# Performance work log

Measured on AMD Instinct MI355X. Metric: run time of the kernel, lower is better.

The kernel has to match this reference:

```python
import jax, jax.numpy as jnp
import numpy as np

DIM = 1024
HEADS = 16
HEAD_DIM = DIM // HEADS
WINDOW = 128


def setup_inputs() -> dict:
    key = jax.random.key(0)
    k1, k2, k3, k4 = jax.random.split(key, 4)
    B, T = 2, 2048
    x = jax.random.normal(k1, (B, T, DIM), dtype=jnp.float32)
    # nn.Linear(dim, 3*dim, bias=False): weight [3*dim, dim]; y = x @ W.T
    W_qkv = jax.random.normal(k2, (3 * DIM, DIM), dtype=jnp.float32) * (1.0 / np.sqrt(DIM))
    W_proj = jax.random.normal(k3, (DIM, DIM), dtype=jnp.float32) * (1.0 / np.sqrt(DIM))
    b_proj = jax.random.normal(k4, (DIM,), dtype=jnp.float32) * 0.01
    return {"x": x, "W_qkv": W_qkv, "W_proj": W_proj, "b_proj": b_proj}


def reference(x, W_qkv, W_proj, b_proj) -> jnp.ndarray:
    B, T, C = x.shape
    scale = HEAD_DIM ** -0.5
    qkv = jnp.einsum('btc,oc->bto', x, W_qkv)  # [B,T,3*D]
    qkv = qkv.reshape(B, T, 3, HEADS, HEAD_DIM)
    qkv = jnp.transpose(qkv, (2, 0, 3, 1, 4))  # [3,B,H,T,hd]
    q, k, v = qkv[0], qkv[1], qkv[2]
    # sliding-window mask: attend iff |i-j| <= WINDOW
    idx = jnp.arange(T)
    mask = jnp.abs(idx[:, None] - idx[None, :]) <= WINDOW  # [T,T]
    scores = jnp.einsum('bhqd,bhkd->bhqk', q, k) * scale  # [B,H,T,T]
    scores = jnp.where(mask[None, None], scores, jnp.finfo(scores.dtype).min)
    attn = jax.nn.softmax(scores, axis=-1)
    out = jnp.einsum('bhqk,bhkd->bhqd', attn, v)  # [B,H,T,hd]
    out = jnp.transpose(out, (0, 2, 1, 3)).reshape(B, T, C)
    return jnp.einsum('btc,oc->bto', out, W_proj) + b_proj
```

## Files before the change

kernel.cpp:

```cpp
#include <hip/hip_runtime.h>
#include <hip/hip_bf16.h>
#include <cstdint>
#include <cstddef>

#define DIMC 1024
#define HEADS 16
#define HD 64
#define WINDOW 128
#define BB 2
#define TT 2048
#define NTOK (BB*TT)
#define QKVN (3*DIMC)

typedef __bf16 bf16;
typedef __bf16 bf16x8 __attribute__((ext_vector_type(8)));
typedef __bf16 bf16x4 __attribute__((ext_vector_type(4)));
typedef float f32x4 __attribute__((ext_vector_type(4)));
typedef unsigned int u32;

typedef const __attribute__((address_space(1))) u32* gp1_t;
typedef __attribute__((address_space(3))) u32* lp3_t;

__device__ __forceinline__ void gload16(const void* g, void* l) {
  __builtin_amdgcn_global_load_lds((gp1_t)g, (lp3_t)l, 16, 0, 0);
}

__device__ __forceinline__ u32 lds_u32(const void* p) {
  return (u32)(uintptr_t)(__attribute__((address_space(3))) const void*)p;
}

__device__ __forceinline__ void BAR() {
  asm volatile("" ::: "memory");
  __builtin_amdgcn_s_barrier();
  asm volatile("" ::: "memory");
}

__global__ void cast3_kernel(const float* __restrict__ x,
                             const float* __restrict__ wq,
                             const float* __restrict__ wp,
                             bf16* __restrict__ xo,
                             bf16* __restrict__ wqo,
                             bf16* __restrict__ wpo) {
  const int NX = NTOK * DIMC / 4;
  const int NQ = QKVN * DIMC / 4;
  const int NP = DIMC * DIMC / 4;
  const int total = NX + NQ + NP;
  typedef float float4v __attribute__((ext_vector_type(4)));
  for (int i = blockIdx.x * blockDim.x + threadIdx.x; i < total;
       i += gridDim.x * blockDim.x) {
    const float4v* src; bf16* dst; int j;
    if (i < NX)            { src = (const float4v*)x;  dst = xo;  j = i; }
    else if (i < NX + NQ)  { src = (const float4v*)wq; dst = wqo; j = i - NX; }
    else                   { src = (const float4v*)wp; dst = wpo; j = i - NX - NQ; }
    float4v v = src[j];
    bf16x4 o;
    o[0] = (bf16)v[0]; o[1] = (bf16)v[1]; o[2] = (bf16)v[2]; o[3] = (bf16)v[3];
    ((bf16x4*)dst)[j] = o;
  }
}

__device__ __forceinline__ bf16x8 lds_frag(const bf16* base, int row, int colb) {
  const char* p = (const char*)base + row * 128 + (colb ^ ((row & 7) << 4));
  return *(const bf16x8*)p;
}

__global__ __launch_bounds__(512, 2) void gemm_qkv_kernel(
    const bf16* __restrict__ A, const bf16* __restrict__ Bw,
    bf16* __restrict__ C) {
  constexpr int NT = 16;
  __shared__ bf16 Al[2][128 * 64];
  __shared__ bf16 Bl[2][192 * 64];

  const int tid = threadIdx.x;
  const int w = tid >> 6, l = tid & 63;
  const int wm = w >> 2, wn = w & 3;
  const int lr = l & 15, lg = l >> 4;

  const int bid = blockIdx.x;
  const int x = bid & 7, i = bid >> 3;
  const int bm = 8 * (x >> 1) + (i & 7);
  const int bn = 8 * (x & 1) + (i >> 3);

  const char* Ag = (const char*)A + (size_t)(bm * 128) * 2048;
  const char* Bg = (const char*)Bw + (size_t)(bn * 192) * 2048;

  auto stageA = [&](bf16* lds, int kt) {
#pragma unroll
    for (int i2 = 0; i2 < 2; i2++) {
      const int R0 = w * 16 + i2 * 8;
      const int r = R0 + (l >> 3);
      const char* src = Ag + (size_t)r * 2048 + kt * 128
                        + (((l & 7) * 16) ^ ((r & 7) << 4));
      gload16(src, lds + R0 * 64);
    }
  };
  auto stageB = [&](bf16* lds, int kt) {
#pragma unroll
    for (int i2 = 0; i2 < 3; i2++) {
      const int R0 = w * 24 + i2 * 8;
      const int r = R0 + (l >> 3);
      const char* src = Bg + (size_t)r * 2048 + kt * 128
                        + (((l & 7) * 16) ^ ((r & 7) << 4));
      gload16(src, lds + R0 * 64);
    }
  };

  stageA(Al[0], 0); stageB(Bl[0], 0);
  stageA(Al[1], 1); stageB(Bl[1], 1);
  asm volatile("s_waitcnt vmcnt(5)" ::: "memory");
  BAR();

  f32x4 acc[4][3] = {};

  for (int kt = 0; kt < NT; ++kt) {
    const bf16* Ac = Al[kt & 1];
    const bf16* Bc = Bl[kt & 1];

    bf16x8 af[4][2], bf[3][2];
#pragma unroll
    for (int m = 0; m < 4; m++)
#pragma unroll
      for (int kk = 0; kk < 2; kk++)
        af[m][kk] = lds_frag(Ac, wm * 64 + m * 16 + lr, kk * 64 + lg * 16);
#pragma unroll
    for (int n = 0; n < 3; n++)
#pragma unroll
      for (int kk = 0; kk < 2; kk++)
        bf[n][kk] = lds_frag(Bc, wn * 48 + n * 16 + lr, kk * 64 + lg * 16);

    asm volatile("s_waitcnt lgkmcnt(0)" ::: "memory");
    __builtin_amdgcn_sched_barrier(0);
    BAR();

    if (kt + 2 < NT) {
      stageA(Al[kt & 1], kt + 2);
      stageB(Bl[kt & 1], kt + 2);
    }

    __builtin_amdgcn_s_setprio(1);
#pragma unroll
    for (int kk = 0; kk < 2; kk++)
#pragma unroll
      for (int m = 0; m < 4; m++)
#pragma unroll
        for (int n = 0; n < 3; n++)
          acc[m][n] = __builtin_amdgcn_mfma_f32_16x16x32_bf16(
              af[m][kk], bf[n][kk], acc[m][n], 0, 0, 0);
    __builtin_amdgcn_s_setprio(0);

    if (kt < NT - 2) asm volatile("s_waitcnt vmcnt(5)" ::: "memory");
    else             asm volatile("s_waitcnt vmcnt(0)" ::: "memory");
    BAR();
  }

#pragma unroll
  for (int m = 0; m < 4; m++) {
    const int row = bm * 128 + wm * 64 + m * 16 + lg * 4;
#pragma unroll
    for (int n = 0; n < 3; n++) {
      const int col = bn * 192 + wn * 48 + n * 16 + lr;
#pragma unroll
      for (int j = 0; j < 4; j++)
        C[(size_t)(row + j) * QKVN + col] = (bf16)acc[m][n][j];
    }
  }
}

__global__ __launch_bounds__(512, 2) void gemm_proj_kernel(
    const bf16* __restrict__ A, const bf16* __restrict__ Bw,
    float* __restrict__ Cf, const float* __restrict__ bias) {
  constexpr int NT = 16;
  __shared__ bf16 Al[2][128 * 64];
  __shared__ bf16 Bl[2][64 * 64];

  const int tid = threadIdx.x;
  const int w = tid >> 6, l = tid & 63;
  const int wm = w >> 1, wn = w & 1;
  const int lr = l & 15, lg = l >> 4;

  const int bid = blockIdx.x;
  const int x = bid & 7, i = bid >> 3;
  const int bm = 8 * (x >> 1) + (i & 7);
  const int bn = 8 * (x & 1) + (i >> 3);

  const char* Ag = (const char*)A + (size_t)(bm * 128) * 2048;
  const char* Bg = (const char*)Bw + (size_t)(bn * 64) * 2048;

  auto stageA = [&](bf16* lds, int kt) {
#pragma unroll
    for (int i2 = 0; i2 < 2; i2++) {
      const int R0 = w * 16 + i2 * 8;
      const int r = R0 + (l >> 3);
      const char* src = Ag + (size_t)r * 2048 + kt * 128
                        + (((l & 7) * 16) ^ ((r & 7) << 4));
      gload16(src, lds + R0 * 64);
    }
  };
  auto stageB = [&](bf16* lds, int kt) {
    const int R0 = w * 8;
    const int r = R0 + (l >> 3);
    const char* src = Bg + (size_t)r * 2048 + kt * 128
                      + (((l & 7) * 16) ^ ((r & 7) << 4));
    gload16(src, lds + R0 * 64);
  };

  stageA(Al[0], 0); stageB(Bl[0], 0);
  stageA(Al[1], 1); stageB(Bl[1], 1);
  asm volatile("s_waitcnt vmcnt(3)" ::: "memory");
  BAR();

  f32x4 acc[2][2] = {};

  for (int kt = 0; kt < NT; ++kt) {
    const bf16* Ac = Al[kt & 1];
    const bf16* Bc = Bl[kt & 1];

    bf16x8 af[2][2], bf[2][2];
#pragma unroll
    for (int m = 0; m < 2; m++)
#pragma unroll
      for (int kk = 0; kk < 2; kk++)
        af[m][kk] = lds_frag(Ac, wm * 32 + m * 16 + lr, kk * 64 + lg * 16);
#pragma unroll
    for (int n = 0; n < 2; n++)
#pragma unroll
      for (int kk = 0; kk < 2; kk++)
        bf[n][kk] = lds_frag(Bc, wn * 32 + n * 16 + lr, kk * 64 + lg * 16);

    asm volatile("s_waitcnt lgkmcnt(0)" ::: "memory");
    __builtin_amdgcn_sched_barrier(0);
    BAR();

    if (kt + 2 < NT) {
      stageA(Al[kt & 1], kt + 2);
      stageB(Bl[kt & 1], kt + 2);
    }

    __builtin_amdgcn_s_setprio(1);
#pragma unroll
    for (int kk = 0; kk < 2; kk++)
#pragma unroll
      for (int m = 0; m < 2; m++)
#pragma unroll
        for (int n = 0; n < 2; n++)
          acc[m][n] = __builtin_amdgcn_mfma_f32_16x16x32_bf16(
              af[m][kk], bf[n][kk], acc[m][n], 0, 0, 0);
    __builtin_amdgcn_s_setprio(0);

    if (kt < NT - 2) asm volatile("s_waitcnt vmcnt(3)" ::: "memory");
    else             asm volatile("s_waitcnt vmcnt(0)" ::: "memory");
    BAR();
  }

#pragma unroll
  for (int m = 0; m < 2; m++) {
    const int row = bm * 128 + wm * 32 + m * 16 + lg * 4;
#pragma unroll
    for (int n = 0; n < 2; n++) {
      const int col = bn * 64 + wn * 32 + n * 16 + lr;
#pragma unroll
      for (int j = 0; j < 4; j++)
        Cf[(size_t)(row + j) * DIMC + col] = acc[m][n][j] + bias[col];
    }
  }
}

__global__ __launch_bounds__(512, 4) void attn_kernel(const bf16* __restrict__ qkv,
                                                      bf16* __restrict__ out) {
  __shared__ bf16 Kl[3][64 * 64];
  __shared__ bf16 Vl[3][64 * 64];

  const int tid = threadIdx.x, w = tid >> 6, l = tid & 63;
  const int bid = blockIdx.x;
  const int x = bid & 7, ii = bid >> 3;
  const int bh = x * 4 + (ii >> 4);
  const int qb = ii & 15;
  const int b = bh >> 4, h = bh & 15;
  const int q0 = qb * 128;
  const int lr = l & 15, lg = l >> 4;
  const float SC = 0.18033688011f;

  const char* qkv_b = (const char*)qkv + (size_t)(b * TT) * (QKVN * 2);

  size_t koff; u32 kdst;
  {
    const int R0 = 8 * w;
    const int r = R0 + (l >> 3);
    const int colb = (((l & 7) * 16) ^ (((l >> 3) & 7) << 4));
    koff = (size_t)r * (QKVN * 2) + (DIMC + h * HD) * 2 + colb;
    kdst = (u32)(R0 * 64);
  }
  size_t voff; u32 vdst;
  {
    const int c = tid;
    const int t = c >> 3, w_ = c & 7;
    const int kv = (t & 15) * 4 + (w_ >> 1);
    const int d  = (t >> 4) * 16 + (w_ & 1) * 8;
    voff = (size_t)kv * (QKVN * 2) + (2 * DIMC + h * HD + d) * 2;
    vdst = (u32)(w * 512);
  }

  auto stage = [&](int buf, int kb) {
    const char* rowb = qkv_b + (size_t)(kb * 64) * (QKVN * 2);
    gload16(rowb + koff, &Kl[buf][kdst]);
    gload16(rowb + voff, &Vl[buf][vdst]);
  };

  bf16x8 qf[2];
  {
    const bf16* qp = qkv + (size_t)(b * TT + q0 + w * 16 + lr) * QKVN + h * HD + lg * 8;
    qf[0] = *(const bf16x8*)qp;
    qf[1] = *(const bf16x8*)(qp + 32);
  }

  f32x4 Oa[4] = {};
  float mrow = -1e30f, lrow = 0.f;

  int kb0 = 2 * qb - 2; if (kb0 < 0) kb0 = 0;
  int kb1 = 2 * qb + 3; if (kb1 > 31) kb1 = 31;

  stage(0, kb0);
  stage(1, kb0 + 1);
  asm volatile("s_waitcnt vmcnt(2)" ::: "memory");
  BAR();

  for (int kb = kb0; kb <= kb1; ++kb) {
    const int c = (kb - kb0) % 3;
    if (kb + 2 <= kb1) stage((c + 2) % 3, kb + 2);

    const bf16* Kb = &Kl[c][0];
    f32x4 Sa[4] = {};
#pragma unroll
    for (int kf = 0; kf < 2; kf++)
#pragma unroll
      for (int nf = 0; nf < 4; nf++) {
        const char* kp = (const char*)Kb + (nf * 16 + lr) * 128
                         + ((kf * 64 + lg * 16) ^ ((lr & 7) << 4));
        bf16x8 kfr = *(const bf16x8*)kp;
        Sa[nf] = __builtin_amdgcn_mfma_f32_16x16x32_bf16(kfr, qf[kf], Sa[nf], 0, 0, 0);
      }

    bf16x4 tr0[4][2], tr1[4][2];
    {
      const u32 vbase = lds_u32(&Vl[c][0]) + l * 8;
#pragma unroll
      for (int nf = 0; nf < 4; nf++)
#pragma unroll
        for (int kf = 0; kf < 2; kf++) {
          const u32 a = vbase + (u32)((nf * 16 + kf * 8) * 128);
          asm volatile("ds_read_b64_tr_b16 %0, %1"
                       : "=v"(tr0[nf][kf]) : "v"(a));
          asm volatile("ds_read_b64_tr_b16 %0, %1 offset:512"
                       : "=v"(tr1[nf][kf]) : "v"(a));
        }
    }

    const int kvb = kb * 64;
    const int qrow = q0 + w * 16 + lr;
    float mblk = -1e30f;
#pragma unroll
    for (int nf = 0; nf < 4; nf++)
#pragma unroll
      for (int j = 0; j < 4; j++) {
        int kv = kvb + nf * 16 + lg * 4 + j;
        int dq = qrow - kv;
        float s = Sa[nf][j] * SC;
        if (dq > WINDOW || dq < -WINDOW) s = -1e30f;
        Sa[nf][j] = s;
        mblk = fmaxf(mblk, s);
      }
    mblk = fmaxf(mblk, __shfl_xor(mblk, 16));
    mblk = fmaxf(mblk, __shfl_xor(mblk, 32));

    if (!__all(mblk <= mrow + 8.f)) {
      float mn = fmaxf(mrow, mblk);
      float sc = exp2f(mrow - mn);
      mrow = mn;
      lrow *= sc;
#pragma unroll
      for (int j = 0; j < 4; j++) {
        float so = __shfl(sc, lg * 4 + j);
#pragma unroll
        for (int nf = 0; nf < 4; nf++) Oa[nf][j] *= so;
      }
    }

    float rsum = 0.f;
#pragma unroll
    for (int nf = 0; nf < 4; nf++)
#pragma unroll
      for (int j = 0; j < 4; j++) {
        float e = exp2f(Sa[nf][j] - mrow);
        Sa[nf][j] = e;
        rsum += e;
      }
    rsum += __shfl_xor(rsum, 16);
    rsum += __shfl_xor(rsum, 32);
    lrow += rsum;

    bf16x8 pa[2];
#pragma unroll
    for (int kf = 0; kf < 2; kf++)
#pragma unroll
      for (int e = 0; e < 4; e++) {
        pa[kf][e]     = (bf16)Sa[2 * kf][e];
        pa[kf][e + 4] = (bf16)Sa[2 * kf + 1][e];
      }

    asm volatile("s_waitcnt lgkmcnt(0)" ::: "memory");
    __builtin_amdgcn_sched_barrier(0);
#pragma unroll
    for (int nf = 0; nf < 4; nf++)
#pragma unroll
      for (int kf = 0; kf < 2; kf++) {
        bf16x8 vb;
#pragma unroll
        for (int e = 0; e < 4; e++) {
          vb[e]     = tr0[nf][kf][e];
          vb[e + 4] = tr1[nf][kf][e];
        }
        Oa[nf] = __builtin_amdgcn_mfma_f32_16x16x32_bf16(pa[kf], vb, Oa[nf], 0, 0, 0);
      }

    if (kb < kb1) {
      if (kb + 2 <= kb1) asm volatile("s_waitcnt vmcnt(2)" ::: "memory");
      else               asm volatile("s_waitcnt vmcnt(0)" ::: "memory");
    }
    BAR();
  }

  float lo[4];
#pragma unroll
  for (int j = 0; j < 4; j++) lo[j] = __shfl(lrow, lg * 4 + j);
#pragma unroll
  for (int nf = 0; nf < 4; nf++) {
#pragma unroll
    for (int j = 0; j < 4; j++) {
      int q = q0 + w * 16 + lg * 4 + j;
      int d = nf * 16 + lr;
      out[(size_t)(b * TT + q) * DIMC + h * HD + d] = (bf16)(Oa[nf][j] / lo[j]);
    }
  }
}

extern "C" void kernel_launch(void* const* d_in, const int* in_sizes, int n_in,
                              void* d_out, int out_size, void* d_ws, size_t ws_size,
                              hipStream_t stream) {
  const float* x     = (const float*)d_in[0];
  const float* Wqkv  = (const float*)d_in[1];
  const float* Wproj = (const float*)d_in[2];
  const float* bproj = (const float*)d_in[3];
  float* out = (float*)d_out;

  char* ws = (char*)d_ws;
  bf16* xb   = (bf16*)(ws);
  bf16* wqb  = (bf16*)(ws + 8388608);
  bf16* wpb  = (bf16*)(ws + 14680064);
  bf16* qkvb = (bf16*)(ws + 16777216);
  bf16* aob  = (bf16*)(ws + 41943040);

  cast3_kernel<<<2048, 256, 0, stream>>>(x, Wqkv, Wproj, xb, wqb, wpb);
  gemm_qkv_kernel<<<512, 512, 0, stream>>>(xb, wqb, qkvb);
  attn_kernel<<<512, 512, 0, stream>>>(qkvb, aob);
  gemm_proj_kernel<<<512, 512, 0, stream>>>(aob, wpb, out, bproj);
}
```

Measured before the change: 76.02 us.

## Fuse weight fp32-to-bf16 conversion into GEMM B-tile loading

The separate cast kernel now converts only x. Both GEMMs load fp32 weight tiles into registers, convert them to bf16 and write them swizzled into LDS, with the next tile's global load issued during the current MFMA phase. This removes a cast pass over 16 MB of fp32 weights and the bf16 weight buffers, but each weight tile is now read as fp32 by many blocks. It also adds register pressure and replaces the async global_load_lds path for B with an explicit register round-trip and different vmcnt waits.

```diff
diff --git a/kernel.cpp b/kernel.cpp
--- a/kernel.cpp
+++ b/kernel.cpp
@@ -16,6 +16,7 @@
 typedef __bf16 bf16x8 __attribute__((ext_vector_type(8)));
 typedef __bf16 bf16x4 __attribute__((ext_vector_type(4)));
 typedef float f32x4 __attribute__((ext_vector_type(4)));
+typedef float float4v __attribute__((ext_vector_type(4)));
 typedef unsigned int u32;
 
 typedef const __attribute__((address_space(1))) u32* gp1_t;
@@ -35,27 +36,15 @@
   asm volatile("" ::: "memory");
 }
 
-__global__ void cast3_kernel(const float* __restrict__ x,
-                             const float* __restrict__ wq,
-                             const float* __restrict__ wp,
-                             bf16* __restrict__ xo,
-                             bf16* __restrict__ wqo,
-                             bf16* __restrict__ wpo) {
+__global__ void castx_kernel(const float* __restrict__ x,
+                             bf16* __restrict__ xo) {
   const int NX = NTOK * DIMC / 4;
-  const int NQ = QKVN * DIMC / 4;
-  const int NP = DIMC * DIMC / 4;
-  const int total = NX + NQ + NP;
-  typedef float float4v __attribute__((ext_vector_type(4)));
-  for (int i = blockIdx.x * blockDim.x + threadIdx.x; i < total;
+  for (int i = blockIdx.x * blockDim.x + threadIdx.x; i < NX;
        i += gridDim.x * blockDim.x) {
-    const float4v* src; bf16* dst; int j;
-    if (i < NX)            { src = (const float4v*)x;  dst = xo;  j = i; }
-    else if (i < NX + NQ)  { src = (const float4v*)wq; dst = wqo; j = i - NX; }
-    else                   { src = (const float4v*)wp; dst = wpo; j = i - NX - NQ; }
-    float4v v = src[j];
+    float4v v = ((const float4v*)x)[i];
     bf16x4 o;
     o[0] = (bf16)v[0]; o[1] = (bf16)v[1]; o[2] = (bf16)v[2]; o[3] = (bf16)v[3];
-    ((bf16x4*)dst)[j] = o;
+    ((bf16x4*)xo)[i] = o;
   }
 }
 
@@ -65,7 +54,7 @@
 }
 
 __global__ __launch_bounds__(512, 2) void gemm_qkv_kernel(
-    const bf16* __restrict__ A, const bf16* __restrict__ Bw,
+    const bf16* __restrict__ A, const float* __restrict__ Wq,
     bf16* __restrict__ C) {
   constexpr int NT = 16;
   __shared__ bf16 Al[2][128 * 64];
@@ -82,7 +71,7 @@
   const int bn = 8 * (x & 1) + (i >> 3);
 
   const char* Ag = (const char*)A + (size_t)(bm * 128) * 2048;
-  const char* Bg = (const char*)Bw + (size_t)(bn * 192) * 2048;
+  const float* Bg = Wq + (size_t)(bn * 192) * 1024;
 
   auto stageA = [&](bf16* lds, int kt) {
 #pragma unroll
@@ -94,20 +83,37 @@
       gload16(src, lds + R0 * 64);
     }
   };
-  auto stageB = [&](bf16* lds, int kt) {
+
+  float br[24];
+  auto loadB = [&](int kt) {
 #pragma unroll
     for (int i2 = 0; i2 < 3; i2++) {
-      const int R0 = w * 24 + i2 * 8;
-      const int r = R0 + (l >> 3);
-      const char* src = Bg + (size_t)r * 2048 + kt * 128
-                        + (((l & 7) * 16) ^ ((r & 7) << 4));
-      gload16(src, lds + R0 * 64);
-    }
-  };
-
-  stageA(Al[0], 0); stageB(Bl[0], 0);
-  stageA(Al[1], 1); stageB(Bl[1], 1);
-  asm volatile("s_waitcnt vmcnt(5)" ::: "memory");
+      const int r = w * 24 + i2 * 8 + (l >> 3);
+      const float* src = Bg + (size_t)r * 1024 + kt * 64 + (l & 7) * 8;
+      float4v v0 = *(const float4v*)src;
+      float4v v1 = *(const float4v*)(src + 4);
+#pragma unroll
+      for (int e = 0; e < 4; e++) { br[i2 * 8 + e] = v0[e]; br[i2 * 8 + 4 + e] = v1[e]; }
+    }
+  };
+  auto writeB = [&](bf16* lds) {
+#pragma unroll
+    for (int i2 = 0; i2 < 3; i2++) {
+      const int r = w * 24 + i2 * 8 + (l >> 3);
+      bf16x8 o;
+#pragma unroll
+      for (int e = 0; e < 8; e++) o[e] = (bf16)br[i2 * 8 + e];
+      *(bf16x8*)((char*)lds + r * 128 + (((l & 7) * 16) ^ ((r & 7) << 4))) = o;
+    }
+  };
+
+  loadB(0);
+  stageA(Al[0], 0); stageA(Al[1], 1);
+  asm volatile("s_waitcnt vmcnt(4)" ::: "memory");
+  writeB(Bl[0]);
+  loadB(1);
+  asm volatile("s_waitcnt vmcnt(8)" ::: "memory");
+  asm volatile("s_waitcnt lgkmcnt(0)" ::: "memory");
   BAR();
 
   f32x4 acc[4][3] = {};
@@ -132,10 +138,13 @@
     __builtin_amdgcn_sched_barrier(0);
     BAR();
 
-    if (kt + 2 < NT) {
-      stageA(Al[kt & 1], kt + 2);
-      stageB(Bl[kt & 1], kt + 2);
-    }
+    if (kt + 2 < NT) stageA(Al[kt & 1], kt + 2);
+    if (kt + 1 < NT) {
+      if (kt + 2 < NT) asm volatile("s_waitcnt vmcnt(2)" ::: "memory");
+      else             asm volatile("s_waitcnt vmcnt(0)" ::: "memory");
+      writeB(Bl[(kt + 1) & 1]);
+    }
+    if (kt + 2 < NT) loadB(kt + 2);
 
     __builtin_amdgcn_s_setprio(1);
 #pragma unroll
@@ -148,8 +157,7 @@
               af[m][kk], bf[n][kk], acc[m][n], 0, 0, 0);
     __builtin_amdgcn_s_setprio(0);
 
-    if (kt < NT - 2) asm volatile("s_waitcnt vmcnt(5)" ::: "memory");
-    else             asm volatile("s_waitcnt vmcnt(0)" ::: "memory");
+    asm volatile("s_waitcnt lgkmcnt(0)" ::: "memory");
     BAR();
   }
 
@@ -167,7 +175,7 @@
 }
 
 __global__ __launch_bounds__(512, 2) void gemm_proj_kernel(
-    const bf16* __restrict__ A, const bf16* __restrict__ Bw,
+    const bf16* __restrict__ A, const float* __restrict__ Wp,
     float* __restrict__ Cf, const float* __restrict__ bias) {
   constexpr int NT = 16;
   __shared__ bf16 Al[2][128 * 64];
@@ -184,7 +192,7 @@
   const int bn = 8 * (x & 1) + (i >> 3);
 
   const char* Ag = (const char*)A + (size_t)(bm * 128) * 2048;
-  const char* Bg = (const char*)Bw + (size_t)(bn * 64) * 2048;
+  const float* Bg = Wp + (size_t)(bn * 64) * 1024;
 
   auto stageA = [&](bf16* lds, int kt) {
 #pragma unroll
@@ -196,17 +204,31 @@
       gload16(src, lds + R0 * 64);
     }
   };
-  auto stageB = [&](bf16* lds, int kt) {
-    const int R0 = w * 8;
-    const int r = R0 + (l >> 3);
-    const char* src = Bg + (size_t)r * 2048 + kt * 128
-                      + (((l & 7) * 16) ^ ((r & 7) << 4));
-    gload16(src, lds + R0 * 64);
-  };
-
-  stageA(Al[0], 0); stageB(Bl[0], 0);
-  stageA(Al[1], 1); stageB(Bl[1], 1);
-  asm volatile("s_waitcnt vmcnt(3)" ::: "memory");
+
+  float br[8];
+  auto loadB = [&](int kt) {
+    const int r = w * 8 + (l >> 3);
+    const float* src = Bg + (size_t)r * 1024 + kt * 64 + (l & 7) * 8;
+    float4v v0 = *(const float4v*)src;
+    float4v v1 = *(const float4v*)(src + 4);
+#pragma unroll
+    for (int e = 0; e < 4; e++) { br[e] = v0[e]; br[4 + e] = v1[e]; }
+  };
+  auto writeB = [&](bf16* lds) {
+    const int r = w * 8 + (l >> 3);
+    bf16x8 o;
+#pragma unroll
+    for (int e = 0; e < 8; e++) o[e] = (bf16)br[e];
+    *(bf16x8*)((char*)lds + r * 128 + (((l & 7) * 16) ^ ((r & 7) << 4))) = o;
+  };
+
+  loadB(0);
+  stageA(Al[0], 0); stageA(Al[1], 1);
+  asm volatile("s_waitcnt vmcnt(4)" ::: "memory");
+  writeB(Bl[0]);
+  loadB(1);
+  asm volatile("s_waitcnt vmcnt(4)" ::: "memory");
+  asm volatile("s_waitcnt lgkmcnt(0)" ::: "memory");
   BAR();
 
   f32x4 acc[2][2] = {};
@@ -231,10 +253,13 @@
     __builtin_amdgcn_sched_barrier(0);
     BAR();
 
-    if (kt + 2 < NT) {
-      stageA(Al[kt & 1], kt + 2);
-      stageB(Bl[kt & 1], kt + 2);
-    }
+    if (kt + 2 < NT) stageA(Al[kt & 1], kt + 2);
+    if (kt + 1 < NT) {
+      if (kt + 2 < NT) asm volatile("s_waitcnt vmcnt(2)" ::: "memory");
+      else             asm volatile("s_waitcnt vmcnt(0)" ::: "memory");
+      writeB(Bl[(kt + 1) & 1]);
+    }
+    if (kt + 2 < NT) loadB(kt + 2);
 
     __builtin_amdgcn_s_setprio(1);
 #pragma unroll
@@ -247,8 +272,7 @@
               af[m][kk], bf[n][kk], acc[m][n], 0, 0, 0);
     __builtin_amdgcn_s_setprio(0);
 
-    if (kt < NT - 2) asm volatile("s_waitcnt vmcnt(3)" ::: "memory");
-    else             asm volatile("s_waitcnt vmcnt(0)" ::: "memory");
+    asm volatile("s_waitcnt lgkmcnt(0)" ::: "memory");
     BAR();
   }
 
@@ -454,13 +478,11 @@
 
   char* ws = (char*)d_ws;
   bf16* xb   = (bf16*)(ws);
-  bf16* wqb  = (bf16*)(ws + 8388608);
-  bf16* wpb  = (bf16*)(ws + 14680064);
-  bf16* qkvb = (bf16*)(ws + 16777216);
-  bf16* aob  = (bf16*)(ws + 41943040);
-
-  cast3_kernel<<<2048, 256, 0, stream>>>(x, Wqkv, Wproj, xb, wqb, wpb);
-  gemm_qkv_kernel<<<512, 512, 0, stream>>>(xb, wqb, qkvb);
+  bf16* qkvb = (bf16*)(ws + 8388608);
+  bf16* aob  = (bf16*)(ws + 33554432);
+
+  castx_kernel<<<1024, 256, 0, stream>>>(x, xb);
+  gemm_qkv_kernel<<<512, 512, 0, stream>>>(xb, Wqkv, qkvb);
   attn_kernel<<<512, 512, 0, stream>>>(qkvb, aob);
-  gemm_proj_kernel<<<512, 512, 0, stream>>>(aob, wpb, out, bproj);
-}
+  gemm_proj_kernel<<<512, 512, 0, stream>>>(aob, Wproj, out, bproj);
+}
```

Result: slower. 87.50 us (+15.1%).
